# Optimization experiments

Measured on AMD Instinct MI355X. Metric: run time of the kernel, lower is better.

The kernel has to match this reference:

```python
import jax, jax.numpy as jnp
import numpy as np

DIM_X = 100   # equation.dim_x
DIM_Y = 1     # equation.dim_y
DIM_D = 100   # equation.dim_d
DIM_H = 512   # dim_h
T_END = 1.0   # equation.T
BN_EPS = 1e-5
SQRT2 = float(np.sqrt(2.0))


def _linear_init(k, fan_in, fan_out):
    lim = 1.0 / np.sqrt(fan_in)
    kw, kb = jax.random.split(k)
    W = jax.random.uniform(kw, (fan_in, fan_out), minval=-lim, maxval=lim, dtype=jnp.float32)
    b = jax.random.uniform(kb, (fan_out,), minval=-lim, maxval=lim, dtype=jnp.float32)
    return W, b


def setup_inputs() -> dict:
    key = jax.random.key(0)
    ks = jax.random.split(key, 6)
    W1, b1 = _linear_init(ks[0], DIM_X + 1, DIM_H)
    W2, b2 = _linear_init(ks[1], DIM_H, DIM_H)
    W3, b3 = _linear_init(ks[2], DIM_H, DIM_H)
    W4, b4 = _linear_init(ks[3], DIM_H, DIM_Y * DIM_D)
    # y_0 = guess_y_0[0]*l + guess_y_0[1]*(1-l), l~U(0,1); guesses (0,1) -> y_0~U(0,1)
    y_0 = jax.random.uniform(ks[4], (DIM_Y,), dtype=jnp.float32)
    x_0 = jnp.zeros((DIM_X,), dtype=jnp.float32)  # equation.x_0
    g1 = jnp.ones((DIM_H,), jnp.float32); be1 = jnp.zeros((DIM_H,), jnp.float32)
    g2 = jnp.ones((DIM_H,), jnp.float32); be2 = jnp.zeros((DIM_H,), jnp.float32)
    return dict(y_0=y_0, W1=W1, b1=b1, W2=W2, b2=b2, W3=W3, b3=b3, W4=W4, b4=b4,
                g1=g1, be1=be1, g2=g2, be2=be2, x_0=x_0, batch_size=4096, N=64)


def reference(y_0, W1, b1, W2, b2, W3, b3, W4, b4, g1, be1, g2, be2, x_0, batch_size, N):
    dt = T_END / N
    sqrt_dt = float(np.sqrt(dt))

    def bn(h, g, be):  # training-mode BatchNorm1d: biased batch stats
        m = jnp.mean(h, axis=0)
        v = jnp.mean(jnp.square(h - m), axis=0)
        return g * (h - m) * jax.lax.rsqrt(v + BN_EPS) + be

    def get_z(x, t):
        h = jnp.concatenate([x, jnp.full((x.shape[0], 1), t, x.dtype)], axis=1)
        h = jax.nn.gelu(h @ W1 + b1, approximate=False)
        h = bn(jax.nn.gelu(h @ W2 + b2, approximate=False), g1, be1)
        h = bn(jax.nn.gelu(h @ W3 + b3, approximate=False), g2, be2)
        return (h @ W4 + b4).reshape(-1, DIM_Y, DIM_D)  # [B, dy, dd]

    x = jnp.broadcast_to(x_0, (batch_size, DIM_X))
    y = jnp.broadcast_to(y_0, (batch_size, DIM_Y))
    ts = jnp.arange(N, dtype=jnp.float32) * dt
    keys = jax.random.split(jax.random.key(42), N)

    def step(carry, inp):
        x, y = carry
        t, k = inp
        z = get_z(x, t)
        dW = jax.random.normal(k, (x.shape[0], DIM_D), dtype=x.dtype) * sqrt_dt
        # b(t,x,y)=0, sigma(t,x)=sqrt(2)*I  =>  x += sqrt(2)*dW
        x = x + SQRT2 * dW
        # f(t,x,y,z) = -0.5*||z||^2 (per dim_y row); z@dW contraction over dim_d
        f = -0.5 * jnp.sum(z * z, axis=2)                 # [B, dy]
        y = y - f * dt + jnp.einsum('byd,bd->by', z, dW)  # [B, dy]
        return (x, y), None

    (x, y), _ = jax.lax.scan(step, (x, y), (ts, keys))
    return x, y
```

## Files before the change

kernel.cpp:

```cpp
#include <hip/hip_runtime.h>
#include <stdint.h>

#define B 4096
#define DX 100
#define H 512
#define DD 100
#define NSTEPS 64
#define KIN 128
#define N4 128
#define NBLK 256
#define NTHR 512

typedef short bf8 __attribute__((ext_vector_type(8)));
typedef float f32x4 __attribute__((ext_vector_type(4)));

__device__ __forceinline__ ushort f2bf(float f) {
  uint32_t u = __float_as_uint(f);
  u += 0x7fffu + ((u >> 16) & 1u);
  return (ushort)(u >> 16);
}
__device__ __forceinline__ float bf2f(ushort h) {
  return __uint_as_float((uint32_t)h << 16);
}
__device__ __forceinline__ f32x4 mfma16(bf8 a, bf8 b, f32x4 c) {
  return __builtin_amdgcn_mfma_f32_16x16x32_bf16(a, b, c, 0, 0, 0);
}

__device__ __forceinline__ int aload_i(int* p) {
  return __hip_atomic_load(p, __ATOMIC_RELAXED, __HIP_MEMORY_SCOPE_AGENT);
}
__device__ __forceinline__ float aload_f(const float* p) {
  return __hip_atomic_load((float*)p, __ATOMIC_RELAXED, __HIP_MEMORY_SCOPE_AGENT);
}

__device__ __forceinline__ void tf2x32(uint32_t k0, uint32_t k1,
                                       uint32_t x0, uint32_t x1,
                                       uint32_t& o0, uint32_t& o1)
{
  uint32_t ks2 = 0x1BD11BDAu ^ k0 ^ k1;
  x0 += k0; x1 += k1;
#define RND(r) { x0 += x1; x1 = (x1 << (r)) | (x1 >> (32 - (r))); x1 ^= x0; }
  RND(13) RND(15) RND(26) RND(6)   x0 += k1;  x1 += ks2 + 1u;
  RND(17) RND(29) RND(16) RND(24)  x0 += ks2; x1 += k0  + 2u;
  RND(13) RND(15) RND(26) RND(6)   x0 += k0;  x1 += k1  + 3u;
  RND(17) RND(29) RND(16) RND(24)  x0 += k1;  x1 += ks2 + 4u;
  RND(13) RND(15) RND(26) RND(6)   x0 += ks2; x1 += k0  + 5u;
#undef RND
  o0 = x0; o1 = x1;
}
__device__ __forceinline__ void step_keys(int step, uint32_t& k0, uint32_t& k1)
{
  tf2x32(0u, 42u, 0u, (uint32_t)step, k0, k1);
}
__device__ __forceinline__ uint32_t jax_bits(uint32_t k0, uint32_t k1, uint32_t m)
{
  uint32_t a, b;
  tf2x32(k0, k1, 0u, m, a, b);
  return a ^ b;
}

__device__ __forceinline__ float jax_normal_from_bits(uint32_t bits)
{
  float f = __uint_as_float((bits >> 9) | 0x3f800000u) - 1.0f;
  const float lo = -0.99999994f;
  float u = fmaxf(lo, f * 2.0f + lo);
  float w = -log1pf(-u * u);
  float p;
  if (w < 5.0f) {
    w -= 2.5f;
    p =          2.81022636e-08f;
    p = fmaf(p, w, 3.43273939e-07f);
    p = fmaf(p, w, -3.5233877e-06f);
    p = fmaf(p, w, -4.39150654e-06f);
    p = fmaf(p, w, 0.00021858087f);
    p = fmaf(p, w, -0.00125372503f);
    p = fmaf(p, w, -0.00417768164f);
    p = fmaf(p, w, 0.246640727f);
    p = fmaf(p, w, 1.50140941f);
  } else {
    w = sqrtf(w) - 3.0f;
    p =          -0.000200214257f;
    p = fmaf(p, w, 0.000100950558f);
    p = fmaf(p, w, 0.00134934322f);
    p = fmaf(p, w, -0.00367342844f);
    p = fmaf(p, w, 0.00573950773f);
    p = fmaf(p, w, -0.0076224613f);
    p = fmaf(p, w, 0.00943887047f);
    p = fmaf(p, w, 1.00167406f);
    p = fmaf(p, w, 2.83297682f);
  }
  return 1.4142135623730951f * (p * u);
}

__device__ __forceinline__ float gelu(float v)
{
  return 0.5f * v * (1.0f + erff(v * 0.7071067811865475f));
}

__global__ void k_prep(const float* __restrict__ W1, const float* __restrict__ W2,
                       const float* __restrict__ W3, const float* __restrict__ W4,
                       ushort* __restrict__ w1t, ushort* __restrict__ w2t,
                       ushort* __restrict__ w3t, ushort* __restrict__ w4t)
{
  int gid = blockIdx.x * blockDim.x + threadIdx.x;
  int stride = gridDim.x * blockDim.x;
  for (int i = gid; i < H * KIN; i += stride) {
    int c = i >> 7, k = i & (KIN - 1);
    w1t[i] = f2bf(k < 101 ? W1[k * H + c] : 0.0f);
  }
  for (int i = gid; i < H * H; i += stride) {
    int c = i >> 9, k = i & (H - 1);
    w2t[i] = f2bf(W2[k * H + c]);
    w3t[i] = f2bf(W3[k * H + c]);
  }
  for (int i = gid; i < N4 * H; i += stride) {
    int c = i >> 9, k = i & (H - 1);
    w4t[i] = f2bf(c < DD ? W4[k * DD + c] : 0.0f);
  }
}


__global__ void k_init_chunk(const float* __restrict__ y0, const float* __restrict__ x0,
                             float* __restrict__ x_run, float* __restrict__ y,
                             float* __restrict__ bn)
{
  int gid = blockIdx.x * blockDim.x + threadIdx.x;
  int stride = gridDim.x * blockDim.x;
  for (int i = gid; i < B * DX; i += stride) x_run[i] = x0[i % DX];
  for (int i = gid; i < B; i += stride) y[i] = y0[0];
  for (int i = gid; i < NSTEPS * 4 * H; i += stride) bn[i] = 0.0f;
}

__global__ void k_xs(float* __restrict__ x_run, ushort* __restrict__ xs,
                     float* __restrict__ xout, int s0, int Sc)
{
  int gid = blockIdx.x * blockDim.x + threadIdx.x;
  int row = gid >> 7, col = gid & 127;
  const float dt = 1.0f / NSTEPS;
  if (col < DX) {
    float xr = x_run[row * DX + col];
    uint32_t m = (uint32_t)(row * DD + col);
    for (int t = 0; t < Sc; ++t) {
      xs[t * (B * KIN) + row * KIN + col] = f2bf(xr);
      uint32_t k0, k1;
      step_keys(s0 + t, k0, k1);
      float dW = 0.125f * jax_normal_from_bits(jax_bits(k0, k1, m));
      xr += 1.4142135623730951f * dW;
    }
    x_run[row * DX + col] = xr;
    if (s0 + Sc == NSTEPS) xout[row * DX + col] = xr;
  } else {
    for (int t = 0; t < Sc; ++t)
      xs[t * (B * KIN) + row * KIN + col] =
          (col == DX) ? f2bf((float)(s0 + t) * dt) : (ushort)0;
  }
}

__global__ __launch_bounds__(256, 4) void kL1(
    const ushort* __restrict__ xs, const ushort* __restrict__ w1t,
    const float* __restrict__ b1, ushort* __restrict__ ga)
{
  __shared__ ushort xt[64][136];
  const int tid = threadIdx.x;
  const int mb = blockIdx.x >> 3, nb = blockIdx.x & 7;
  const int base = mb * 64;

  for (int i = tid; i < 64 * 16; i += 256) {
    int r = i >> 4, kk = (i & 15) * 8;
    *(bf8*)&xt[r][kk] = *(const bf8*)&xs[(base + r) * KIN + kk];
  }
  __syncthreads();

  const int w = tid >> 6, lane = tid & 63, lr = lane & 15, lg = lane >> 4;
  const int col = nb * 64 + w * 16 + lr;
  f32x4 acc[4];
#pragma unroll
  for (int mi = 0; mi < 4; mi++) acc[mi] = (f32x4)(0.0f);
#pragma unroll
  for (int ks = 0; ks < 4; ks++) {
    bf8 b = *(const bf8*)(w1t + col * KIN + ks * 32 + lg * 8);
#pragma unroll
    for (int mi = 0; mi < 4; mi++) {
      bf8 a = *(const bf8*)&xt[mi * 16 + lr][ks * 32 + lg * 8];
      acc[mi] = mfma16(a, b, acc[mi]);
    }
  }
  float bb = b1[col];
#pragma unroll
  for (int mi = 0; mi < 4; mi++)
#pragma unroll
    for (int r = 0; r < 4; r++)
      ga[(base + mi * 16 + lg * 4 + r) * H + col] = f2bf(gelu(acc[mi][r] + bb));
}

__global__ __launch_bounds__(256, 4) void kL2(
    const ushort* __restrict__ ga, const ushort* __restrict__ w2t,
    const float* __restrict__ b2, ushort* __restrict__ gb,
    float* __restrict__ bn, int s0)
{
  __shared__ ushort at[64][264];
  const int tid = threadIdx.x;
  const int mb = blockIdx.x >> 3, nb = blockIdx.x & 7;
  const int base = mb * 64;
  float* bns = bn + (s0 + (mb >> 6)) * 4 * H;
  float* bnq = bns + H;
  const int w = tid >> 6, lane = tid & 63, lr = lane & 15, lg = lane >> 4;
  const int col = nb * 64 + w * 16 + lr;

  f32x4 acc[4];
#pragma unroll
  for (int mi = 0; mi < 4; mi++) acc[mi] = (f32x4)(0.0f);

#pragma unroll
  for (int c = 0; c < 2; c++) {
    if (c) __syncthreads();
    for (int i = tid; i < 2048; i += 256) {
      int r = i >> 5, kk = (i & 31) * 8;
      *(bf8*)&at[r][kk] = *(const bf8*)&ga[(base + r) * H + c * 256 + kk];
    }
    __syncthreads();
#pragma unroll
    for (int ks = 0; ks < 8; ks++) {
      bf8 b = *(const bf8*)(w2t + col * H + c * 256 + ks * 32 + lg * 8);
#pragma unroll
      for (int mi = 0; mi < 4; mi++) {
        bf8 a = *(const bf8*)&at[mi * 16 + lr][ks * 32 + lg * 8];
        acc[mi] = mfma16(a, b, acc[mi]);
      }
    }
  }

  float bb = b2[col], s = 0.0f, q = 0.0f;
#pragma unroll
  for (int mi = 0; mi < 4; mi++)
#pragma unroll
    for (int r = 0; r < 4; r++) {
      float v = gelu(acc[mi][r] + bb);
      gb[(base + mi * 16 + lg * 4 + r) * H + col] = f2bf(v);
      s += v; q += v * v;
    }
  s += __shfl_xor(s, 16); s += __shfl_xor(s, 32);
  q += __shfl_xor(q, 16); q += __shfl_xor(q, 32);
  if (lane < 16) { unsafeAtomicAdd(&bns[col], s); unsafeAtomicAdd(&bnq[col], q); }
}

__global__ __launch_bounds__(256, 4) void kL3(
    const ushort* __restrict__ gb, float* __restrict__ bn, int s0,
    const float* __restrict__ gamma, const float* __restrict__ beta,
    const ushort* __restrict__ w3t, const float* __restrict__ b3,
    ushort* __restrict__ ga)
{
  __shared__ float sc[H], sh[H];
  __shared__ ushort at[64][264];
  const int tid = threadIdx.x;
  const int mb = blockIdx.x >> 3, nb = blockIdx.x & 7;
  const int base = mb * 64;
  float* bn1s = bn + (s0 + (mb >> 6)) * 4 * H;
  float* bn1q = bn1s + H;
  float* bn2s = bn1s + 2 * H;
  float* bn2q = bn1s + 3 * H;
  const int w = tid >> 6, lane = tid & 63, lr = lane & 15, lg = lane >> 4;
  const int col = nb * 64 + w * 16 + lr;

  for (int c = tid; c < H; c += 256) {
    float m = bn1s[c] * (1.0f / B);
    float v = bn1q[c] * (1.0f / B) - m * m;
    float s2_ = gamma[c] * rsqrtf(v + 1e-5f);
    sc[c] = s2_; sh[c] = beta[c] - m * s2_;
  }

  f32x4 acc[4];
#pragma unroll
  for (int mi = 0; mi < 4; mi++) acc[mi] = (f32x4)(0.0f);

#pragma unroll
  for (int c = 0; c < 2; c++) {
    __syncthreads();
    for (int i = tid; i < 4096; i += 256) {
      int r = i >> 6, k4 = (i & 63) * 4, gk = c * 256 + k4;
      ushort4 gv = *(const ushort4*)&gb[(base + r) * H + gk];
      ushort4 o;
      o.x = f2bf(fmaf(bf2f(gv.x), sc[gk + 0], sh[gk + 0]));
      o.y = f2bf(fmaf(bf2f(gv.y), sc[gk + 1], sh[gk + 1]));
      o.z = f2bf(fmaf(bf2f(gv.z), sc[gk + 2], sh[gk + 2]));
      o.w = f2bf(fmaf(bf2f(gv.w), sc[gk + 3], sh[gk + 3]));
      *(ushort4*)&at[r][k4] = o;
    }
    __syncthreads();
#pragma unroll
    for (int ks = 0; ks < 8; ks++) {
      bf8 b = *(const bf8*)(w3t + col * H + c * 256 + ks * 32 + lg * 8);
#pragma unroll
      for (int mi = 0; mi < 4; mi++) {
        bf8 a = *(const bf8*)&at[mi * 16 + lr][ks * 32 + lg * 8];
        acc[mi] = mfma16(a, b, acc[mi]);
      }
    }
  }

  float bb = b3[col], s = 0.0f, q = 0.0f;
#pragma unroll
  for (int mi = 0; mi < 4; mi++)
#pragma unroll
    for (int r = 0; r < 4; r++) {
      float v = gelu(acc[mi][r] + bb);
      ga[(base + mi * 16 + lg * 4 + r) * H + col] = f2bf(v);
      s += v; q += v * v;
    }
  s += __shfl_xor(s, 16); s += __shfl_xor(s, 32);
  q += __shfl_xor(q, 16); q += __shfl_xor(q, 32);
  if (lane < 16) { unsafeAtomicAdd(&bn2s[col], s); unsafeAtomicAdd(&bn2q[col], q); }
}

__global__ __launch_bounds__(512, 4) void kL4(
    const ushort* __restrict__ ga, const float* __restrict__ bn, int s0,
    const float* __restrict__ gamma, const float* __restrict__ beta,
    const ushort* __restrict__ w4t, const float* __restrict__ b4,
    float* __restrict__ y)
{
  __shared__ float sc[H], sh[H];
  __shared__ ushort at16[16 * 520];
  __shared__ float ys1[8][16], ys2[8][16];
  const int tid = threadIdx.x;
  const int sb = blockIdx.x >> 8;
  const int s = s0 + sb;
  const int lb = (blockIdx.x & 255) * 16;
  const int rbase = sb * B + lb;
  const float dt = 1.0f / NSTEPS;
  const float* bn2s = bn + s * 4 * H + 2 * H;
  const float* bn2q = bn2s + H;

  for (int c = tid; c < H; c += 512) {
    float m = bn2s[c] * (1.0f / B);
    float v = bn2q[c] * (1.0f / B) - m * m;
    float s2_ = gamma[c] * rsqrtf(v + 1e-5f);
    sc[c] = s2_; sh[c] = beta[c] - m * s2_;
  }
  __syncthreads();
  for (int i = tid; i < 2048; i += 512) {
    int r = i >> 7, k4 = (i & 127) * 4;
    ushort4 gv = *(const ushort4*)&ga[(rbase + r) * H + k4];
    ushort4 o;
    o.x = f2bf(fmaf(bf2f(gv.x), sc[k4 + 0], sh[k4 + 0]));
    o.y = f2bf(fmaf(bf2f(gv.y), sc[k4 + 1], sh[k4 + 1]));
    o.z = f2bf(fmaf(bf2f(gv.z), sc[k4 + 2], sh[k4 + 2]));
    o.w = f2bf(fmaf(bf2f(gv.w), sc[k4 + 3], sh[k4 + 3]));
    *(ushort4*)&at16[r * 520 + k4] = o;
  }
  __syncthreads();

  const int w = tid >> 6, lane = tid & 63, lr = lane & 15, lg = lane >> 4;
  const int col = w * 16 + lr;
  f32x4 acc = (f32x4)(0.0f);
#pragma unroll
  for (int ks = 0; ks < 16; ks++) {
    bf8 a = *(const bf8*)&at16[lr * 520 + ks * 32 + lg * 8];
    bf8 b = *(const bf8*)(w4t + col * H + ks * 32 + lg * 8);
    acc = mfma16(a, b, acc);
  }

  uint32_t k0, k1;
  step_keys(s, k0, k1);
  float zz[4] = {0, 0, 0, 0}, zw[4] = {0, 0, 0, 0};
  if (col < DD) {
    float bb = b4[col];
#pragma unroll
    for (int r = 0; r < 4; r++) {
      int lrow = lb + lg * 4 + r;
      float z = acc[r] + bb;
      uint32_t m = (uint32_t)lrow * (uint32_t)DD + (uint32_t)col;
      float dW = 0.125f * jax_normal_from_bits(jax_bits(k0, k1, m));
      zz[r] = z * z;
      zw[r] = z * dW;
    }
  }
#pragma unroll
  for (int r = 0; r < 4; r++) {
    zz[r] += __shfl_xor(zz[r], 1); zz[r] += __shfl_xor(zz[r], 2);
    zz[r] += __shfl_xor(zz[r], 4); zz[r] += __shfl_xor(zz[r], 8);
    zw[r] += __shfl_xor(zw[r], 1); zw[r] += __shfl_xor(zw[r], 2);
    zw[r] += __shfl_xor(zw[r], 4); zw[r] += __shfl_xor(zw[r], 8);
  }
  if (lr == 0) {
#pragma unroll
    for (int r = 0; r < 4; r++) {
      ys1[w][lg * 4 + r] = zz[r];
      ys2[w][lg * 4 + r] = zw[r];
    }
  }
  __syncthreads();
  if (tid < 16) {
    float s1 = 0.0f, s2_ = 0.0f;
#pragma unroll
    for (int i = 0; i < 8; i++) { s1 += ys1[i][tid]; s2_ += ys2[i][tid]; }
    unsafeAtomicAdd(&y[lb + tid], 0.5f * dt * s1 + s2_);
  }
}


__device__ __forceinline__ void gbar(int* cnt, int* gen, int mode)
{
  if (mode) __builtin_amdgcn_fence(__ATOMIC_RELEASE, "agent");
  __syncthreads();
  if (threadIdx.x == 0) {
    int g = aload_i(gen);
    int a = __hip_atomic_fetch_add(cnt, 1, __ATOMIC_RELAXED, __HIP_MEMORY_SCOPE_AGENT);
    if (a == NBLK - 1) {
      __hip_atomic_store(cnt, 0, __ATOMIC_RELAXED, __HIP_MEMORY_SCOPE_AGENT);
      __hip_atomic_store(gen, g + 1, __ATOMIC_RELAXED, __HIP_MEMORY_SCOPE_AGENT);
    } else {
      while (aload_i(gen) == g) __builtin_amdgcn_s_sleep(2);
    }
  }
  __syncthreads();
  if (mode) __builtin_amdgcn_fence(__ATOMIC_ACQUIRE, "agent");
  else      asm volatile("buffer_inv" ::: "memory");
}

__global__ void k_init_coop(const float* __restrict__ y0, const float* __restrict__ x0,
                            float* __restrict__ x, float* __restrict__ y,
                            float* __restrict__ bn, int* __restrict__ bar)
{
  int gid = blockIdx.x * blockDim.x + threadIdx.x;
  int stride = gridDim.x * blockDim.x;
  for (int i = gid; i < B * DX; i += stride) x[i] = x0[i % DX];
  for (int i = gid; i < B; i += stride) y[i] = y0[0];
  for (int i = gid; i < NSTEPS * 4 * H; i += stride) bn[i] = 0.0f;
  if (gid < 32) bar[gid] = 0;
}

__device__ __forceinline__ void l1_sec(const ushort* xt, const ushort* __restrict__ w1t,
                                       const float* __restrict__ b1,
                                       ushort* __restrict__ h1g,
                                       int base, int w, int lr, int lg)
{
  f32x4 a1[4];
#pragma unroll
  for (int t = 0; t < 4; t++) a1[t] = (f32x4)(0.0f);
#pragma unroll
  for (int ks = 0; ks < 4; ks++) {
    bf8 a = *(const bf8*)&xt[lr * 136 + ks * 32 + lg * 8];
#pragma unroll
    for (int t = 0; t < 4; t++) {
      int cc = w * 64 + t * 16 + lr;
      bf8 bfr = *(const bf8*)(w1t + cc * KIN + ks * 32 + lg * 8);
      a1[t] = mfma16(a, bfr, a1[t]);
    }
  }
#pragma unroll
  for (int t = 0; t < 4; t++) {
    int cc = w * 64 + t * 16 + lr;
    float bb = b1[cc];
#pragma unroll
    for (int r = 0; r < 4; r++)
      h1g[(base + lg * 4 + r) * H + cc] = f2bf(gelu(a1[t][r] + bb));
  }
}

__global__ void __launch_bounds__(NTHR, 2) k_steps(
    const ushort* __restrict__ w1t, const float* __restrict__ b1,
    const ushort* __restrict__ w2t, const float* __restrict__ b2,
    const ushort* __restrict__ w3t, const float* __restrict__ b3,
    const ushort* __restrict__ w4t, const float* __restrict__ b4,
    const float* __restrict__ ga1, const float* __restrict__ be1,
    const float* __restrict__ ga2, const float* __restrict__ be2,
    ushort* __restrict__ g1, ushort* __restrict__ g2h,
    float* __restrict__ bn, float* __restrict__ x, float* __restrict__ y,
    int* __restrict__ bar)
{
  __shared__ ushort smem[64 * 264];
  __shared__ float sc[H], sh[H];
  __shared__ float ys1[8][16], ys2[8][16];
  __shared__ int dsh[2];

  const int tid = threadIdx.x;
  const int w = tid >> 6, lane = tid & 63, lr = lane & 15, lg = lane >> 4;
  const float dt = 1.0f / NSTEPS;
  int* cnt = bar; int* gen = bar + 1;
  int* bins = bar + 2;
  int* gcnt = bar + 18;

  int sgs, mode;
  {
    if (tid == 0) {
      uint32_t xcc = __builtin_amdgcn_s_getreg(20 | (31 << 11)) & 15u;
      int j = __hip_atomic_fetch_add(&bins[xcc], 1, __ATOMIC_RELAXED, __HIP_MEMORY_SCOPE_AGENT);
      dsh[0] = (int)xcc; dsh[1] = j;
    }
    gbar(cnt, gen, 1);
    if (tid == 0) {
      int ok = 1;
      for (int k = 0; k < 8; k++)  ok &= (aload_i(&bins[k]) == 32);
      for (int k = 8; k < 16; k++) ok &= (aload_i(&bins[k]) == 0);
      if (ok) { dsh[0] = dsh[0] * 32 + dsh[1]; dsh[1] = 0; }
      else {
        dsh[0] = __hip_atomic_fetch_add(gcnt, 1, __ATOMIC_RELAXED, __HIP_MEMORY_SCOPE_AGENT);
        dsh[1] = 1;
      }
    }
    __syncthreads();
    sgs = dsh[0]; mode = dsh[1];
  }
  const int mb = sgs >> 2, q = sgs & 3;
  const int cbase = sgs * 16;

  {
    ushort* xt = smem;
    for (int i = tid; i < 16 * KIN; i += NTHR) {
      int r = i >> 7, k = i & (KIN - 1);
      xt[r * 136 + k] = (k < DX) ? f2bf(x[(cbase + r) * DX + k]) : (ushort)0;
    }
    __syncthreads();
    l1_sec(xt, w1t, b1, g2h, cbase, w, lr, lg);
  }
  gbar(cnt, gen, mode);

  for (int s = 0; s < NSTEPS; ++s) {
    float* bn1s = bn + s * 4 * H;
    float* bn1q = bn1s + H;
    float* bn2s = bn1s + 2 * H;
    float* bn2q = bn1s + 3 * H;

    {
      const int col = q * 128 + w * 16 + lr;
      f32x4 acc[4];
#pragma unroll
      for (int mi = 0; mi < 4; mi++) acc[mi] = (f32x4)(0.0f);
#pragma unroll
      for (int c = 0; c < 2; c++) {
        if (c) __syncthreads();
        for (int i = tid; i < 2048; i += NTHR) {
          int r = i >> 5, kk = (i & 31) * 8;
          *(bf8*)&smem[r * 264 + kk] = *(const bf8*)&g2h[(mb * 64 + r) * H + c * 256 + kk];
        }
        __syncthreads();
#pragma unroll
        for (int ks = 0; ks < 8; ks++) {
          bf8 b = *(const bf8*)(w2t + col * H + c * 256 + ks * 32 + lg * 8);
#pragma unroll
          for (int mi = 0; mi < 4; mi++) {
            bf8 a = *(const bf8*)&smem[(mi * 16 + lr) * 264 + ks * 32 + lg * 8];
            acc[mi] = mfma16(a, b, acc[mi]);
          }
        }
      }
      float bb = b2[col], ssum = 0.0f, qsum = 0.0f;
#pragma unroll
      for (int mi = 0; mi < 4; mi++)
#pragma unroll
        for (int r = 0; r < 4; r++) {
          float v = gelu(acc[mi][r] + bb);
          g1[(mb * 64 + mi * 16 + lg * 4 + r) * H + col] = f2bf(v);
          ssum += v; qsum += v * v;
        }
      ssum += __shfl_xor(ssum, 16); ssum += __shfl_xor(ssum, 32);
      qsum += __shfl_xor(qsum, 16); qsum += __shfl_xor(qsum, 32);
      if (lane < 16) { unsafeAtomicAdd(&bn1s[col], ssum); unsafeAtomicAdd(&bn1q[col], qsum); }
    }
    gbar(cnt, gen, mode);

    {
      const int col = q * 128 + w * 16 + lr;
      for (int c = tid; c < H; c += NTHR) {
        float m = aload_f(&bn1s[c]) * (1.0f / B);
        float v = aload_f(&bn1q[c]) * (1.0f / B) - m * m;
        float s2_ = ga1[c] * rsqrtf(v + 1e-5f);
        sc[c] = s2_; sh[c] = be1[c] - m * s2_;
      }
      __syncthreads();
      f32x4 acc[4];
#pragma unroll
      for (int mi = 0; mi < 4; mi++) acc[mi] = (f32x4)(0.0f);
#pragma unroll
      for (int c = 0; c < 2; c++) {
        if (c) __syncthreads();
        for (int i = tid; i < 4096; i += NTHR) {
          int r = i >> 6, k4 = (i & 63) * 4, gk = c * 256 + k4;
          ushort4 gv = *(const ushort4*)&g1[(mb * 64 + r) * H + gk];
          ushort4 o;
          o.x = f2bf(fmaf(bf2f(gv.x), sc[gk + 0], sh[gk + 0]));
          o.y = f2bf(fmaf(bf2f(gv.y), sc[gk + 1], sh[gk + 1]));
          o.z = f2bf(fmaf(bf2f(gv.z), sc[gk + 2], sh[gk + 2]));
          o.w = f2bf(fmaf(bf2f(gv.w), sc[gk + 3], sh[gk + 3]));
          *(ushort4*)&smem[r * 264 + k4] = o;
        }
        __syncthreads();
#pragma unroll
        for (int ks = 0; ks < 8; ks++) {
          bf8 b = *(const bf8*)(w3t + col * H + c * 256 + ks * 32 + lg * 8);
#pragma unroll
          for (int mi = 0; mi < 4; mi++) {
            bf8 a = *(const bf8*)&smem[(mi * 16 + lr) * 264 + ks * 32 + lg * 8];
            acc[mi] = mfma16(a, b, acc[mi]);
          }
        }
      }
      float bb = b3[col], ssum = 0.0f, qsum = 0.0f;
#pragma unroll
      for (int mi = 0; mi < 4; mi++)
#pragma unroll
        for (int r = 0; r < 4; r++) {
          float v = gelu(acc[mi][r] + bb);
          g2h[(mb * 64 + mi * 16 + lg * 4 + r) * H + col] = f2bf(v);
          ssum += v; qsum += v * v;
        }
      ssum += __shfl_xor(ssum, 16); ssum += __shfl_xor(ssum, 32);
      qsum += __shfl_xor(qsum, 16); qsum += __shfl_xor(qsum, 32);
      if (lane < 16) { unsafeAtomicAdd(&bn2s[col], ssum); unsafeAtomicAdd(&bn2q[col], qsum); }
    }
    gbar(cnt, gen, mode);

    {
      ushort* at16 = smem;
      ushort* xt   = smem + 16 * 520;
      for (int c = tid; c < H; c += NTHR) {
        float m = aload_f(&bn2s[c]) * (1.0f / B);
        float v = aload_f(&bn2q[c]) * (1.0f / B) - m * m;
        float s2_ = ga2[c] * rsqrtf(v + 1e-5f);
        sc[c] = s2_; sh[c] = be2[c] - m * s2_;
      }
      __syncthreads();
      for (int i = tid; i < 2048; i += NTHR) {
        int r = i >> 7, k4 = (i & 127) * 4;
        ushort4 gv = *(const ushort4*)&g2h[(cbase + r) * H + k4];
        ushort4 o;
        o.x = f2bf(fmaf(bf2f(gv.x), sc[k4 + 0], sh[k4 + 0]));
        o.y = f2bf(fmaf(bf2f(gv.y), sc[k4 + 1], sh[k4 + 1]));
        o.z = f2bf(fmaf(bf2f(gv.z), sc[k4 + 2], sh[k4 + 2]));
        o.w = f2bf(fmaf(bf2f(gv.w), sc[k4 + 3], sh[k4 + 3]));
        *(ushort4*)&at16[r * 520 + k4] = o;
      }
      __syncthreads();

      const int col = w * 16 + lr;
      f32x4 acc = (f32x4)(0.0f);
#pragma unroll
      for (int ks = 0; ks < 16; ks++) {
        bf8 a = *(const bf8*)&at16[lr * 520 + ks * 32 + lg * 8];
        bf8 b = *(const bf8*)(w4t + col * H + ks * 32 + lg * 8);
        acc = mfma16(a, b, acc);
      }

      uint32_t k0, k1;
      step_keys(s, k0, k1);
      float zz[4] = {0, 0, 0, 0}, zw[4] = {0, 0, 0, 0};
      float tnext = (float)(s + 1) * dt;
      if (col < DD) {
        float bb = b4[col];
#pragma unroll
        for (int r = 0; r < 4; r++) {
          int row = lg * 4 + r, grow = cbase + row;
          float z = acc[r] + bb;
          uint32_t m = (uint32_t)grow * (uint32_t)DD + (uint32_t)col;
          float dW = 0.125f * jax_normal_from_bits(jax_bits(k0, k1, m));
          float xn = x[grow * DX + col] + 1.4142135623730951f * dW;
          x[grow * DX + col] = xn;
          xt[row * 136 + col] = f2bf(xn);
          zz[r] = z * z;
          zw[r] = z * dW;
        }
      } else {
#pragma unroll
        for (int r = 0; r < 4; r++)
          xt[(lg * 4 + r) * 136 + col] = (col == DX) ? f2bf(tnext) : (ushort)0;
      }
#pragma unroll
      for (int r = 0; r < 4; r++) {
        zz[r] += __shfl_xor(zz[r], 1); zz[r] += __shfl_xor(zz[r], 2);
        zz[r] += __shfl_xor(zz[r], 4); zz[r] += __shfl_xor(zz[r], 8);
        zw[r] += __shfl_xor(zw[r], 1); zw[r] += __shfl_xor(zw[r], 2);
        zw[r] += __shfl_xor(zw[r], 4); zw[r] += __shfl_xor(zw[r], 8);
      }
      if (lr == 0) {
#pragma unroll
        for (int r = 0; r < 4; r++) {
          ys1[w][lg * 4 + r] = zz[r];
          ys2[w][lg * 4 + r] = zw[r];
        }
      }
      __syncthreads();
      if (tid < 16) {
        float s1 = 0.0f, s2_ = 0.0f;
#pragma unroll
        for (int i = 0; i < 8; i++) { s1 += ys1[i][tid]; s2_ += ys2[i][tid]; }
        y[cbase + tid] += 0.5f * dt * s1 + s2_;
      }
      if (s < NSTEPS - 1)
        l1_sec(xt, w1t, b1, g2h, cbase, w, lr, lg);
    }
    if (s < NSTEPS - 1) gbar(cnt, gen, mode);
  }
}


extern "C" void kernel_launch(void* const* d_in, const int* in_sizes, int n_in,
                              void* d_out, int out_size, void* d_ws, size_t ws_size,
                              hipStream_t stream)
{
  const float* y0  = (const float*)d_in[0];
  const float* W1  = (const float*)d_in[1];
  const float* b1  = (const float*)d_in[2];
  const float* W2  = (const float*)d_in[3];
  const float* b2  = (const float*)d_in[4];
  const float* W3  = (const float*)d_in[5];
  const float* b3  = (const float*)d_in[6];
  const float* W4  = (const float*)d_in[7];
  const float* b4  = (const float*)d_in[8];
  const float* ga1 = (const float*)d_in[9];
  const float* be1 = (const float*)d_in[10];
  const float* ga2 = (const float*)d_in[11];
  const float* be2 = (const float*)d_in[12];
  const float* x0  = (const float*)d_in[13];

  float* x = (float*)d_out;
  float* y = x + B * DX;

  const size_t fixed_b = (size_t)NSTEPS * 4 * H * 4 + (size_t)B * DX * 4 +
                         (size_t)(H * KIN + H * H + H * H + N4 * H) * 2;
  const size_t per_b = (size_t)B * H * 2 * 2;
  long smax = ((long)ws_size - (long)fixed_b) / (long)per_b;
  int S = (int)(smax < 64 ? smax : 64);

  if (S >= 1) {
    float* bn    = (float*)d_ws;
    float* x_run = bn + NSTEPS * 4 * H;
    ushort* w1t = (ushort*)(x_run + B * DX);
    ushort* w2t = w1t + H * KIN;
    ushort* w3t = w2t + H * H;
    ushort* w4t = w3t + H * H;
    ushort* ga  = w4t + N4 * H;
    ushort* gb  = ga + (size_t)S * B * H;
    ushort* xs  = gb;

    k_init_chunk<<<256, 256, 0, stream>>>(y0, x0, x_run, y, bn);
    k_prep<<<512, 256, 0, stream>>>(W1, W2, W3, W4, w1t, w2t, w3t, w4t);

    for (int s0 = 0; s0 < NSTEPS; s0 += S) {
      int Sc = (NSTEPS - s0 < S) ? (NSTEPS - s0) : S;
      k_xs<<<(B * KIN) / 256, 256, 0, stream>>>(x_run, xs, x, s0, Sc);
      kL1<<<Sc * 512, 256, 0, stream>>>(xs, w1t, b1, ga);
      kL2<<<Sc * 512, 256, 0, stream>>>(ga, w2t, b2, gb, bn, s0);
      kL3<<<Sc * 512, 256, 0, stream>>>(gb, bn, s0, ga1, be1, w3t, b3, ga);
      kL4<<<Sc * 256, 512, 0, stream>>>(ga, bn, s0, ga2, be2, w4t, b4, y);
    }
  } else {
    int*   bar = (int*)d_ws;
    float* bn  = (float*)d_ws + 32;
    ushort* ub  = (ushort*)(bn + NSTEPS * 4 * H);
    ushort* g1  = ub;
    ushort* g2h = g1 + B * H;
    ushort* w1t = g2h + B * H;
    ushort* w2t = w1t + H * KIN;
    ushort* w3t = w2t + H * H;
    ushort* w4t = w3t + H * H;

    k_init_coop<<<256, 256, 0, stream>>>(y0, x0, x, y, bn, bar);
    k_prep<<<512, 256, 0, stream>>>(W1, W2, W3, W4, w1t, w2t, w3t, w4t);

    void* args[] = {
      (void*)&w1t, (void*)&b1, (void*)&w2t, (void*)&b2,
      (void*)&w3t, (void*)&b3, (void*)&w4t, (void*)&b4,
      (void*)&ga1, (void*)&be1, (void*)&ga2, (void*)&be2,
      (void*)&g1, (void*)&g2h, (void*)&bn, (void*)&x, (void*)&y, (void*)&bar
    };
    hipLaunchCooperativeKernel((const void*)k_steps, dim3(NBLK), dim3(NTHR),
                               args, 0, stream);
  }
}
```

Baseline: 1.678 ms.

## Fuse layer-1 GEMM into layer-2 kernel and widen output tiles per block

Layer 1 is now computed inside the layer-2 kernel, and each block regenerates its 64x256 hidden slice into shared memory, so the first activation never goes to global memory. Layers 2 and 3 switch from 64-column to 256-column output tiles per block, giving each wave a 4x4 accumulator grid so A fragments are reused across four column tiles. Layer 4 handles 32 rows per block instead of 16. Because each of the two column-half blocks recomputes the full layer 1, layer-1 work doubles. Larger accumulator sets also lower occupancy, and launch bounds drop from 4 to 2.

```diff
diff --git a/kernel.cpp b/kernel.cpp
--- a/kernel.cpp
+++ b/kernel.cpp
@@ -156,95 +156,101 @@
   }
 }
 
-__global__ __launch_bounds__(256, 4) void kL1(
+__global__ __launch_bounds__(256, 2) void kL12(
     const ushort* __restrict__ xs, const ushort* __restrict__ w1t,
-    const float* __restrict__ b1, ushort* __restrict__ ga)
-{
-  __shared__ ushort xt[64][136];
-  const int tid = threadIdx.x;
-  const int mb = blockIdx.x >> 3, nb = blockIdx.x & 7;
-  const int base = mb * 64;
-
-  for (int i = tid; i < 64 * 16; i += 256) {
-    int r = i >> 4, kk = (i & 15) * 8;
-    *(bf8*)&xt[r][kk] = *(const bf8*)&xs[(base + r) * KIN + kk];
-  }
-  __syncthreads();
-
-  const int w = tid >> 6, lane = tid & 63, lr = lane & 15, lg = lane >> 4;
-  const int col = nb * 64 + w * 16 + lr;
-  f32x4 acc[4];
-#pragma unroll
-  for (int mi = 0; mi < 4; mi++) acc[mi] = (f32x4)(0.0f);
-#pragma unroll
-  for (int ks = 0; ks < 4; ks++) {
-    bf8 b = *(const bf8*)(w1t + col * KIN + ks * 32 + lg * 8);
-#pragma unroll
-    for (int mi = 0; mi < 4; mi++) {
-      bf8 a = *(const bf8*)&xt[mi * 16 + lr][ks * 32 + lg * 8];
-      acc[mi] = mfma16(a, b, acc[mi]);
-    }
-  }
-  float bb = b1[col];
-#pragma unroll
-  for (int mi = 0; mi < 4; mi++)
-#pragma unroll
-    for (int r = 0; r < 4; r++)
-      ga[(base + mi * 16 + lg * 4 + r) * H + col] = f2bf(gelu(acc[mi][r] + bb));
-}
-
-__global__ __launch_bounds__(256, 4) void kL2(
-    const ushort* __restrict__ ga, const ushort* __restrict__ w2t,
+    const float* __restrict__ b1, const ushort* __restrict__ w2t,
     const float* __restrict__ b2, ushort* __restrict__ gb,
     float* __restrict__ bn, int s0)
 {
+  __shared__ ushort xt[64][136];
   __shared__ ushort at[64][264];
   const int tid = threadIdx.x;
-  const int mb = blockIdx.x >> 3, nb = blockIdx.x & 7;
+  const int mb = blockIdx.x >> 1, nb = blockIdx.x & 1;
   const int base = mb * 64;
   float* bns = bn + (s0 + (mb >> 6)) * 4 * H;
   float* bnq = bns + H;
   const int w = tid >> 6, lane = tid & 63, lr = lane & 15, lg = lane >> 4;
-  const int col = nb * 64 + w * 16 + lr;
-
-  f32x4 acc[4];
-#pragma unroll
-  for (int mi = 0; mi < 4; mi++) acc[mi] = (f32x4)(0.0f);
+
+  for (int i = tid; i < 64 * 16; i += 256) {
+    int r = i >> 4, kk = (i & 15) * 8;
+    *(bf8*)&xt[r][kk] = *(const bf8*)&xs[(base + r) * KIN + kk];
+  }
+
+  f32x4 acc[4][4];
+#pragma unroll
+  for (int mi = 0; mi < 4; mi++)
+#pragma unroll
+    for (int t = 0; t < 4; t++) acc[mi][t] = (f32x4)(0.0f);
 
 #pragma unroll
   for (int c = 0; c < 2; c++) {
-    if (c) __syncthreads();
-    for (int i = tid; i < 2048; i += 256) {
-      int r = i >> 5, kk = (i & 31) * 8;
-      *(bf8*)&at[r][kk] = *(const bf8*)&ga[(base + r) * H + c * 256 + kk];
-    }
     __syncthreads();
 #pragma unroll
+    for (int tp = 0; tp < 2; tp++) {
+      f32x4 a1[4][2];
+#pragma unroll
+      for (int mi = 0; mi < 4; mi++) { a1[mi][0] = (f32x4)(0.0f); a1[mi][1] = (f32x4)(0.0f); }
+#pragma unroll
+      for (int ks = 0; ks < 4; ks++) {
+        bf8 af[4];
+#pragma unroll
+        for (int mi = 0; mi < 4; mi++)
+          af[mi] = *(const bf8*)&xt[mi * 16 + lr][ks * 32 + lg * 8];
+#pragma unroll
+        for (int u = 0; u < 2; u++) {
+          int hcol = c * 256 + w * 64 + (tp * 2 + u) * 16 + lr;
+          bf8 b = *(const bf8*)(w1t + hcol * KIN + ks * 32 + lg * 8);
+#pragma unroll
+          for (int mi = 0; mi < 4; mi++) a1[mi][u] = mfma16(af[mi], b, a1[mi][u]);
+        }
+      }
+#pragma unroll
+      for (int u = 0; u < 2; u++) {
+        int lcol = w * 64 + (tp * 2 + u) * 16 + lr;
+        float bb = b1[c * 256 + lcol];
+#pragma unroll
+        for (int mi = 0; mi < 4; mi++)
+#pragma unroll
+          for (int r = 0; r < 4; r++)
+            at[mi * 16 + lg * 4 + r][lcol] = f2bf(gelu(a1[mi][u][r] + bb));
+      }
+    }
+    __syncthreads();
+#pragma unroll
     for (int ks = 0; ks < 8; ks++) {
-      bf8 b = *(const bf8*)(w2t + col * H + c * 256 + ks * 32 + lg * 8);
-#pragma unroll
-      for (int mi = 0; mi < 4; mi++) {
-        bf8 a = *(const bf8*)&at[mi * 16 + lr][ks * 32 + lg * 8];
-        acc[mi] = mfma16(a, b, acc[mi]);
-      }
-    }
-  }
-
-  float bb = b2[col], s = 0.0f, q = 0.0f;
-#pragma unroll
-  for (int mi = 0; mi < 4; mi++)
-#pragma unroll
-    for (int r = 0; r < 4; r++) {
-      float v = gelu(acc[mi][r] + bb);
-      gb[(base + mi * 16 + lg * 4 + r) * H + col] = f2bf(v);
-      s += v; q += v * v;
-    }
-  s += __shfl_xor(s, 16); s += __shfl_xor(s, 32);
-  q += __shfl_xor(q, 16); q += __shfl_xor(q, 32);
-  if (lane < 16) { unsafeAtomicAdd(&bns[col], s); unsafeAtomicAdd(&bnq[col], q); }
-}
-
-__global__ __launch_bounds__(256, 4) void kL3(
+      bf8 af[4];
+#pragma unroll
+      for (int mi = 0; mi < 4; mi++)
+        af[mi] = *(const bf8*)&at[mi * 16 + lr][ks * 32 + lg * 8];
+#pragma unroll
+      for (int t = 0; t < 4; t++) {
+        int col = nb * 256 + w * 64 + t * 16 + lr;
+        bf8 b = *(const bf8*)(w2t + col * H + c * 256 + ks * 32 + lg * 8);
+#pragma unroll
+        for (int mi = 0; mi < 4; mi++) acc[mi][t] = mfma16(af[mi], b, acc[mi][t]);
+      }
+    }
+  }
+
+#pragma unroll
+  for (int t = 0; t < 4; t++) {
+    int col = nb * 256 + w * 64 + t * 16 + lr;
+    float bb = b2[col], s = 0.0f, q = 0.0f;
+#pragma unroll
+    for (int mi = 0; mi < 4; mi++)
+#pragma unroll
+      for (int r = 0; r < 4; r++) {
+        float v = gelu(acc[mi][t][r] + bb);
+        gb[(base + mi * 16 + lg * 4 + r) * H + col] = f2bf(v);
+        s += v; q += v * v;
+      }
+    s += __shfl_xor(s, 16); s += __shfl_xor(s, 32);
+    q += __shfl_xor(q, 16); q += __shfl_xor(q, 32);
+    if (lane < 16) { unsafeAtomicAdd(&bns[col], s); unsafeAtomicAdd(&bnq[col], q); }
+  }
+}
+
+__global__ __launch_bounds__(256, 2) void kL3(
     const ushort* __restrict__ gb, float* __restrict__ bn, int s0,
     const float* __restrict__ gamma, const float* __restrict__ beta,
     const ushort* __restrict__ w3t, const float* __restrict__ b3,
@@ -253,14 +259,13 @@
   __shared__ float sc[H], sh[H];
   __shared__ ushort at[64][264];
   const int tid = threadIdx.x;
-  const int mb = blockIdx.x >> 3, nb = blockIdx.x & 7;
+  const int mb = blockIdx.x >> 1, nb = blockIdx.x & 1;
   const int base = mb * 64;
   float* bn1s = bn + (s0 + (mb >> 6)) * 4 * H;
   float* bn1q = bn1s + H;
   float* bn2s = bn1s + 2 * H;
   float* bn2q = bn1s + 3 * H;
   const int w = tid >> 6, lane = tid & 63, lr = lane & 15, lg = lane >> 4;
-  const int col = nb * 64 + w * 16 + lr;
 
   for (int c = tid; c < H; c += 256) {
     float m = bn1s[c] * (1.0f / B);
@@ -269,9 +274,11 @@
     sc[c] = s2_; sh[c] = beta[c] - m * s2_;
   }
 
-  f32x4 acc[4];
-#pragma unroll
-  for (int mi = 0; mi < 4; mi++) acc[mi] = (f32x4)(0.0f);
+  f32x4 acc[4][4];
+#pragma unroll
+  for (int mi = 0; mi < 4; mi++)
+#pragma unroll
+    for (int t = 0; t < 4; t++) acc[mi][t] = (f32x4)(0.0f);
 
 #pragma unroll
   for (int c = 0; c < 2; c++) {
@@ -289,42 +296,51 @@
     __syncthreads();
 #pragma unroll
     for (int ks = 0; ks < 8; ks++) {
-      bf8 b = *(const bf8*)(w3t + col * H + c * 256 + ks * 32 + lg * 8);
-#pragma unroll
-      for (int mi = 0; mi < 4; mi++) {
-        bf8 a = *(const bf8*)&at[mi * 16 + lr][ks * 32 + lg * 8];
-        acc[mi] = mfma16(a, b, acc[mi]);
-      }
-    }
-  }
-
-  float bb = b3[col], s = 0.0f, q = 0.0f;
-#pragma unroll
-  for (int mi = 0; mi < 4; mi++)
-#pragma unroll
-    for (int r = 0; r < 4; r++) {
-      float v = gelu(acc[mi][r] + bb);
-      ga[(base + mi * 16 + lg * 4 + r) * H + col] = f2bf(v);
-      s += v; q += v * v;
-    }
-  s += __shfl_xor(s, 16); s += __shfl_xor(s, 32);
-  q += __shfl_xor(q, 16); q += __shfl_xor(q, 32);
-  if (lane < 16) { unsafeAtomicAdd(&bn2s[col], s); unsafeAtomicAdd(&bn2q[col], q); }
-}
-
-__global__ __launch_bounds__(512, 4) void kL4(
+      bf8 af[4];
+#pragma unroll
+      for (int mi = 0; mi < 4; mi++)
+        af[mi] = *(const bf8*)&at[mi * 16 + lr][ks * 32 + lg * 8];
+#pragma unroll
+      for (int t = 0; t < 4; t++) {
+        int col = nb * 256 + w * 64 + t * 16 + lr;
+        bf8 b = *(const bf8*)(w3t + col * H + c * 256 + ks * 32 + lg * 8);
+#pragma unroll
+        for (int mi = 0; mi < 4; mi++) acc[mi][t] = mfma16(af[mi], b, acc[mi][t]);
+      }
+    }
+  }
+
+#pragma unroll
+  for (int t = 0; t < 4; t++) {
+    int col = nb * 256 + w * 64 + t * 16 + lr;
+    float bb = b3[col], s = 0.0f, q = 0.0f;
+#pragma unroll
+    for (int mi = 0; mi < 4; mi++)
+#pragma unroll
+      for (int r = 0; r < 4; r++) {
+        float v = gelu(acc[mi][t][r] + bb);
+        ga[(base + mi * 16 + lg * 4 + r) * H + col] = f2bf(v);
+        s += v; q += v * v;
+      }
+    s += __shfl_xor(s, 16); s += __shfl_xor(s, 32);
+    q += __shfl_xor(q, 16); q += __shfl_xor(q, 32);
+    if (lane < 16) { unsafeAtomicAdd(&bn2s[col], s); unsafeAtomicAdd(&bn2q[col], q); }
+  }
+}
+
+__global__ __launch_bounds__(512, 2) void kL4(
     const ushort* __restrict__ ga, const float* __restrict__ bn, int s0,
     const float* __restrict__ gamma, const float* __restrict__ beta,
     const ushort* __restrict__ w4t, const float* __restrict__ b4,
     float* __restrict__ y)
 {
   __shared__ float sc[H], sh[H];
-  __shared__ ushort at16[16 * 520];
-  __shared__ float ys1[8][16], ys2[8][16];
+  __shared__ ushort at[32 * 520];
+  __shared__ float ys1[8][32], ys2[8][32];
   const int tid = threadIdx.x;
-  const int sb = blockIdx.x >> 8;
+  const int sb = blockIdx.x >> 7;
   const int s = s0 + sb;
-  const int lb = (blockIdx.x & 255) * 16;
+  const int lb = (blockIdx.x & 127) * 32;
   const int rbase = sb * B + lb;
   const float dt = 1.0f / NSTEPS;
   const float* bn2s = bn + s * 4 * H + 2 * H;
@@ -337,7 +353,7 @@
     sc[c] = s2_; sh[c] = beta[c] - m * s2_;
   }
   __syncthreads();
-  for (int i = tid; i < 2048; i += 512) {
+  for (int i = tid; i < 32 * 128; i += 512) {
     int r = i >> 7, k4 = (i & 127) * 4;
     ushort4 gv = *(const ushort4*)&ga[(rbase + r) * H + k4];
     ushort4 o;
@@ -345,51 +361,58 @@
     o.y = f2bf(fmaf(bf2f(gv.y), sc[k4 + 1], sh[k4 + 1]));
     o.z = f2bf(fmaf(bf2f(gv.z), sc[k4 + 2], sh[k4 + 2]));
     o.w = f2bf(fmaf(bf2f(gv.w), sc[k4 + 3], sh[k4 + 3]));
-    *(ushort4*)&at16[r * 520 + k4] = o;
+    *(ushort4*)&at[r * 520 + k4] = o;
   }
   __syncthreads();
 
   const int w = tid >> 6, lane = tid & 63, lr = lane & 15, lg = lane >> 4;
   const int col = w * 16 + lr;
-  f32x4 acc = (f32x4)(0.0f);
+  f32x4 acc[2];
+  acc[0] = (f32x4)(0.0f); acc[1] = (f32x4)(0.0f);
 #pragma unroll
   for (int ks = 0; ks < 16; ks++) {
-    bf8 a = *(const bf8*)&at16[lr * 520 + ks * 32 + lg * 8];
     bf8 b = *(const bf8*)(w4t + col * H + ks * 32 + lg * 8);
-    acc = mfma16(a, b, acc);
+#pragma unroll
+    for (int mi = 0; mi < 2; mi++) {
+      bf8 a = *(const bf8*)&at[(mi * 16 + lr) * 520 + ks * 32 + lg * 8];
+      acc[mi] = mfma16(a, b, acc[mi]);
+    }
   }
 
   uint32_t k0, k1;
   step_keys(s, k0, k1);
-  float zz[4] = {0, 0, 0, 0}, zw[4] = {0, 0, 0, 0};
-  if (col < DD) {
-    float bb = b4[col];
+#pragma unroll
+  for (int mi = 0; mi < 2; mi++) {
+    float zz[4] = {0, 0, 0, 0}, zw[4] = {0, 0, 0, 0};
+    if (col < DD) {
+      float bb = b4[col];
+#pragma unroll
+      for (int r = 0; r < 4; r++) {
+        int lrow = lb + mi * 16 + lg * 4 + r;
+        float z = acc[mi][r] + bb;
+        uint32_t m = (uint32_t)lrow * (uint32_t)DD + (uint32_t)col;
+        float dW = 0.125f * jax_normal_from_bits(jax_bits(k0, k1, m));
+        zz[r] = z * z;
+        zw[r] = z * dW;
+      }
+    }
 #pragma unroll
     for (int r = 0; r < 4; r++) {
-      int lrow = lb + lg * 4 + r;
-      float z = acc[r] + bb;
-      uint32_t m = (uint32_t)lrow * (uint32_t)DD + (uint32_t)col;
-      float dW = 0.125f * jax_normal_from_bits(jax_bits(k0, k1, m));
-      zz[r] = z * z;
-      zw[r] = z * dW;
-    }
-  }
-#pragma unroll
-  for (int r = 0; r < 4; r++) {
-    zz[r] += __shfl_xor(zz[r], 1); zz[r] += __shfl_xor(zz[r], 2);
-    zz[r] += __shfl_xor(zz[r], 4); zz[r] += __shfl_xor(zz[r], 8);
-    zw[r] += __shfl_xor(zw[r], 1); zw[r] += __shfl_xor(zw[r], 2);
-    zw[r] += __shfl_xor(zw[r], 4); zw[r] += __shfl_xor(zw[r], 8);
-  }
-  if (lr == 0) {
-#pragma unroll
-    for (int r = 0; r < 4; r++) {
-      ys1[w][lg * 4 + r] = zz[r];
-      ys2[w][lg * 4 + r] = zw[r];
+      zz[r] += __shfl_xor(zz[r], 1); zz[r] += __shfl_xor(zz[r], 2);
+      zz[r] += __shfl_xor(zz[r], 4); zz[r] += __shfl_xor(zz[r], 8);
+      zw[r] += __shfl_xor(zw[r], 1); zw[r] += __shfl_xor(zw[r], 2);
+      zw[r] += __shfl_xor(zw[r], 4); zw[r] += __shfl_xor(zw[r], 8);
+    }
+    if (lr == 0) {
+#pragma unroll
+      for (int r = 0; r < 4; r++) {
+        ys1[w][mi * 16 + lg * 4 + r] = zz[r];
+        ys2[w][mi * 16 + lg * 4 + r] = zw[r];
+      }
     }
   }
   __syncthreads();
-  if (tid < 16) {
+  if (tid < 32) {
     float s1 = 0.0f, s2_ = 0.0f;
 #pragma unroll
     for (int i = 0; i < 8; i++) { s1 += ys1[i][tid]; s2_ += ys2[i][tid]; }
@@ -730,7 +753,7 @@
     ushort* w4t = w3t + H * H;
     ushort* ga  = w4t + N4 * H;
     ushort* gb  = ga + (size_t)S * B * H;
-    ushort* xs  = gb;
+    ushort* xs  = ga;
 
     k_init_chunk<<<256, 256, 0, stream>>>(y0, x0, x_run, y, bn);
     k_prep<<<512, 256, 0, stream>>>(W1, W2, W3, W4, w1t, w2t, w3t, w4t);
@@ -738,10 +761,9 @@
     for (int s0 = 0; s0 < NSTEPS; s0 += S) {
       int Sc = (NSTEPS - s0 < S) ? (NSTEPS - s0) : S;
       k_xs<<<(B * KIN) / 256, 256, 0, stream>>>(x_run, xs, x, s0, Sc);
-      kL1<<<Sc * 512, 256, 0, stream>>>(xs, w1t, b1, ga);
-      kL2<<<Sc * 512, 256, 0, stream>>>(ga, w2t, b2, gb, bn, s0);
-      kL3<<<Sc * 512, 256, 0, stream>>>(gb, bn, s0, ga1, be1, w3t, b3, ga);
-      kL4<<<Sc * 256, 512, 0, stream>>>(ga, bn, s0, ga2, be2, w4t, b4, y);
+      kL12<<<Sc * 128, 256, 0, stream>>>(xs, w1t, b1, w2t, b2, gb, bn, s0);
+      kL3 <<<Sc * 128, 256, 0, stream>>>(gb, bn, s0, ga1, be1, w3t, b3, ga);
+      kL4 <<<Sc * 128, 512, 0, stream>>>(ga, bn, s0, ga2, be2, w4t, b4, y);
     }
   } else {
     int*   bar = (int*)d_ws;
```

Measured after the change: 1.666 ms. No clear change (-0.7%).
